# Kernel tuning notes

Measured on AMD Instinct MI355X. Metric: run time of the kernel, lower is better.

## Reference

```python
import jax, jax.numpy as jnp
import numpy as np
import math

B, D, N, H, NHEADS, NCLS = 4096, 256, 256, 1, 4, 10


def conv(x, w, b, stride, pad):
    y = jax.lax.conv_general_dilated(x, w, (stride, stride), [(pad, pad), (pad, pad)],
                                     dimension_numbers=('NCHW', 'OIHW', 'NCHW'))
    return y + b[None, :, None, None]


def cdist(z, c):
    # z: [B, D], c: [N, D] -> Euclidean distance [B, N]
    d2 = jnp.sum(z * z, -1)[:, None] + jnp.sum(c * c, -1)[None, :] - 2.0 * (z @ c.T)
    return jnp.sqrt(jnp.maximum(d2, 0.0))


def setup_inputs() -> dict:
    key = jax.random.key(0)
    ks = jax.random.split(key, 32)
    s = 0.02
    inp = {
        'x': jax.random.normal(ks[0], (B, 3, 32, 32), jnp.float32),
        'y': jax.random.randint(ks[1], (B,), 0, NCLS),
        'conv1_w': jax.random.normal(ks[2], (32, 3, 5, 5), jnp.float32) * s,
        'conv1_b': jnp.zeros((32,), jnp.float32),
        'conv2_w': jax.random.normal(ks[3], (64, 32, 3, 3), jnp.float32) * s,
        'conv2_b': jnp.zeros((64,), jnp.float32),
        'conv3_w': jax.random.normal(ks[4], (128, 64, 3, 3), jnp.float32) * s,
        'conv3_b': jnp.zeros((128,), jnp.float32),
        'conv4_w': jax.random.normal(ks[5], (256, 128, 3, 3), jnp.float32) * s,
        'conv4_b': jnp.zeros((256,), jnp.float32),
        'enc_w': jax.random.normal(ks[6], (256 * 8 * 8, D), jnp.float32) * s,
        'enc_b': jnp.zeros((D,), jnp.float32),
        'class_emb': jax.random.normal(ks[7], (NCLS, D), jnp.float32),
        'node_emb': jax.random.normal(ks[8], (N_NODES := 1, D), jnp.float32),
        'query_w': jax.random.normal(ks[9], (D, D), jnp.float32) * s,
        'query_b': jnp.zeros((D,), jnp.float32),
        'attn_w': jax.random.normal(ks[10], (D, D * NHEADS), jnp.float32) * s,
        'attn_b': jnp.zeros((D * NHEADS,), jnp.float32),
        'clf_w': jax.random.normal(ks[11], (D * NHEADS, NCLS), jnp.float32) * s,
        'clf_b': jnp.zeros((NCLS,), jnp.float32),
        'node_fc_w': jax.random.normal(ks[12], (D, D), jnp.float32) * s,
        'node_fc_b': jnp.zeros((D,), jnp.float32),
        'protos': jax.random.normal(ks[13], (N, D), jnp.float32),
        'grid_pos': jax.random.normal(ks[14], (N, D), jnp.float32),
        'temp_raw': jnp.array([math.log(0.95 / 0.05)], jnp.float32),
        'gate_logits': jnp.zeros((N,), jnp.float32),
    }
    return inp


def reference(x, y, conv1_w, conv1_b, conv2_w, conv2_b, conv3_w, conv3_b,
              conv4_w, conv4_b, enc_w, enc_b, class_emb, node_emb,
              query_w, query_b, attn_w, attn_b, clf_w, clf_b,
              node_fc_w, node_fc_b, protos, grid_pos, temp_raw, gate_logits):
    # shared encoder: conv stack -> flatten -> linear, 32x32 -> 8x8
    h1 = jax.nn.relu(conv(x, conv1_w, conv1_b, 2, 1))    # [B,32,15,15]
    h2 = jax.nn.relu(conv(h1, conv2_w, conv2_b, 2, 1))   # [B,64,8,8]
    h3 = jax.nn.relu(conv(h2, conv3_w, conv3_b, 1, 1))   # [B,128,8,8]
    h4 = jax.nn.relu(conv(h3, conv4_w, conv4_b, 1, 1))   # [B,256,8,8]
    z0 = h4.reshape(x.shape[0], -1) @ enc_w + enc_b      # [B,D]

    # Node: encoder_fc + SoftSOM (cdist + cdist -> softmax -> gate -> renorm -> blend)
    z = z0 @ node_fc_w + node_fc_b
    temp = jax.nn.sigmoid(temp_raw[0]) * (1.0 - 0.001) + 0.001
    d_total = cdist(z, protos) + cdist(z, grid_pos)      # [B,N]
    w = jax.nn.softmax(-d_total / temp, axis=-1) * jax.nn.sigmoid(gate_logits)[None, :]
    w = w / (w.sum(-1, keepdims=True) + 1e-8)
    blended = w @ protos                                 # [B,D]

    # node attention over n_nodes=1
    topo_stack = blended[:, None, :]                     # [B,1,D]
    query = class_emb[y] @ query_w + query_b             # [B,D]
    proj = (node_emb @ attn_w + attn_b).reshape(node_emb.shape[0], NHEADS, D)  # [n,h,D]
    attn_logits = jnp.einsum('bd,nhd->bhn', query, proj)
    attn_w_ = jax.nn.softmax(attn_logits, axis=-1)
    fused = jnp.einsum('bhn,bnd->bhd', attn_w_, topo_stack).reshape(x.shape[0], NHEADS * D)
    logits = fused @ clf_w + clf_b                       # [B,10]
    return logits
```

## Files before the change

### kernel.cpp

```cpp
#include <hip/hip_runtime.h>
#include <math.h>

#define TPB 256

typedef __attribute__((ext_vector_type(8))) short bf16x8;
typedef __attribute__((ext_vector_type(4))) float f32x4;
typedef __attribute__((ext_vector_type(2))) float f32x2;

#define OFF_PN2   0
#define OFF_GN2   256
#define OFF_GATE  512
#define OFF_TEMP  768
#define OFF_WEFF  1024
#define OFF_W1T   3584
#define OFF_W2T_BYTES 737280ul
#define OFF_W3T_BYTES 786432ul
#define OFF_W4T_BYTES 983040ul
#define OFF_EWT_BYTES 2097152ul
#define OFF_NFWT_BYTES 10485760ul
#define OFF_PJD_BYTES  10616832ul
#define OFF_GJD_BYTES  10747904ul
#define OFF_PTB_BYTES  10878976ul
#define OFF_A_BYTES   12582912ul
#define OFF_B_BYTES   (OFF_A_BYTES + 67108864ul)
#define OFF_Z0_BYTES  (OFF_B_BYTES + 33554432ul)

__device__ __forceinline__ float bf2f(ushort u) {
  return __uint_as_float(((unsigned)u) << 16);
}
__device__ __forceinline__ ushort f2bf(float f) {
  unsigned x = __float_as_uint(f);
  return (ushort)((x + 0x7fffu + ((x >> 16) & 1u)) >> 16);
}
__device__ __forceinline__ unsigned pack2(float a, float b) {
  return (unsigned)f2bf(a) | ((unsigned)f2bf(b) << 16);
}

__device__ __forceinline__ void gload_lds16(const ushort* g, ushort* l) {
  __builtin_amdgcn_global_load_lds(
      (const __attribute__((address_space(1))) unsigned int*)g,
      (__attribute__((address_space(3))) unsigned int*)l, 16, 0, 0);
}

__device__ __forceinline__ float block_sum(float v, float* red) {
  #pragma unroll
  for (int off = 32; off > 0; off >>= 1) v += __shfl_down(v, off, 64);
  int wid = threadIdx.x >> 6;
  __syncthreads();
  if ((threadIdx.x & 63) == 0) red[wid] = v;
  __syncthreads();
  return red[0] + red[1] + red[2] + red[3];
}

__global__ void __launch_bounds__(256) k_setup(const float* __restrict__ protos,
    const float* __restrict__ gridp, const float* __restrict__ gate_logits,
    const float* __restrict__ temp_raw, const float* __restrict__ clf_w,
    float* __restrict__ ws, float* __restrict__ z0) {
  __shared__ float red[4];
  int b = blockIdx.x, t = threadIdx.x;
  #pragma unroll
  for (int u = 0; u < 16; ++u) z0[(size_t)u*65536 + b*256 + t] = 0.f;
  float pv = protos[b*256 + t];
  float gv = gridp [b*256 + t];
  float sp = block_sum(pv*pv, red);
  float sg = block_sum(gv*gv, red);
  if (t == 0) {
    ws[OFF_PN2 + b] = sp;
    ws[OFF_GN2 + b] = sg;
    ws[OFF_GATE + b] = 1.f/(1.f + expf(-gate_logits[b]));
  }
  if (b == 0) {
    for (int i = t; i < 2560; i += TPB) {
      int d = i/10, c = i%10;
      ws[OFF_WEFF + i] = clf_w[d*10+c] + clf_w[(256+d)*10+c]
                       + clf_w[(512+d)*10+c] + clf_w[(768+d)*10+c];
    }
    if (t == 0) {
      float s = 1.f/(1.f + expf(-temp_raw[0]));
      ws[OFF_TEMP] = s*(1.f - 0.001f) + 0.001f;
    }
  }
}

__global__ void __launch_bounds__(256) k_prep(const float* __restrict__ w1,
    const float* __restrict__ w2, const float* __restrict__ w3,
    const float* __restrict__ w4, float* __restrict__ w1t,
    ushort* __restrict__ w2t, ushort* __restrict__ w3t, ushort* __restrict__ w4t) {
  int idx = blockIdx.x*256 + threadIdx.x;
  if (idx < 2400) {
    int tap = idx >> 5, oc = idx & 31;
    w1t[idx] = w1[oc*75 + tap];
  }
  if (idx < 18432) {
    int tap = idx >> 11, r = idx & 2047, oc = r >> 5, ic = r & 31;
    w2t[idx] = f2bf(w2[oc*288 + ic*9 + tap]);
  }
  if (idx < 73728) {
    int tap = idx >> 13, r = idx & 8191, oc = r >> 6, ic = r & 63;
    w3t[idx] = f2bf(w3[oc*576 + ic*9 + tap]);
  }
  if (idx < 294912) {
    int tap = idx >> 15, r = idx & 32767, oc = r >> 7, ic = r & 127;
    w4t[idx] = f2bf(w4[oc*1152 + ic*9 + tap]);
  }
}

__global__ void __launch_bounds__(256) k_prep2(const float* __restrict__ nfw,
    const float* __restrict__ protos, const float* __restrict__ gridp,
    ushort* __restrict__ nfwt, ushort* __restrict__ pjd,
    ushort* __restrict__ gjd, ushort* __restrict__ ptb) {
  int idx = blockIdx.x*256 + threadIdx.x;
  int a = idx >> 8, b = idx & 255;
  nfwt[idx] = f2bf(nfw[b*256 + a]);
  pjd [idx] = f2bf(protos[idx]);
  gjd [idx] = f2bf(gridp[idx]);
  ptb [idx] = f2bf(protos[b*256 + a]);
}

__global__ void __launch_bounds__(256) k_trans(const float* __restrict__ ew,
    ushort* __restrict__ ewt) {
  __shared__ float tile[64][65];
  int kb = blockIdx.x, nb = blockIdx.y, t = threadIdx.x;
  #pragma unroll
  for (int i = 0; i < 16; ++i) {
    int idx = t + i*256, k = idx >> 6, n = idx & 63;
    tile[k][n] = ew[(size_t)(kb*64 + k)*256 + nb*64 + n];
  }
  __syncthreads();
  #pragma unroll
  for (int i = 0; i < 16; ++i) {
    int idx = t + i*256, n = idx >> 6, k = idx & 63;
    ewt[(size_t)(nb*64 + n)*16384 + kb*64 + k] = f2bf(tile[k][n]);
  }
}

__global__ void __launch_bounds__(256) k_conv12(const float* __restrict__ x,
    const float* __restrict__ w1t, const float* __restrict__ b1,
    const ushort* __restrict__ w2t, const float* __restrict__ b2,
    ushort* __restrict__ h2c) {
  __shared__ ushort xs[17*17*40];
  int b = blockIdx.x, t = threadIdx.x;
  for (int i = t; i < 5780; i += TPB) ((unsigned*)xs)[i] = 0u;
  const float* xb = x + (size_t)b*3072;

  if (t < 225) {
    int oy = t/15, ox = t%15;
    f32x2 acc[16];
    #pragma unroll
    for (int o = 0; o < 16; ++o) acc[o] = *(const f32x2*)&b1[2*o];
    for (int ic = 0; ic < 3; ++ic) {
      const int icb = ic*1024;
      #pragma unroll
      for (int ky = 0; ky < 5; ++ky) {
        int iy = 2*oy - 1 + ky;
        bool rok = (unsigned)iy < 32u;
        int rbase = icb + (rok ? iy*32 : 0);
        #pragma unroll
        for (int kx = 0; kx < 5; ++kx) {
          int ix = 2*ox - 1 + kx;
          bool ok = rok && ((unsigned)ix < 32u);
          float xv = xb[rbase + (ok ? ix : 0)];
          xv = ok ? xv : 0.f;
          f32x2 xv2 = {xv, xv};
          const float* wrow = &w1t[(ic*25 + ky*5 + kx)*32];
          #pragma unroll
          for (int g = 0; g < 8; ++g) {
            f32x2 wlo = {wrow[4*g+0], wrow[4*g+1]};
            f32x2 whi = {wrow[4*g+2], wrow[4*g+3]};
            acc[2*g]   += xv2*wlo;
            acc[2*g+1] += xv2*whi;
          }
        }
      }
    }
    unsigned pk[16];
    #pragma unroll
    for (int g = 0; g < 16; ++g)
      pk[g] = pack2(fmaxf(acc[g].x, 0.f), fmaxf(acc[g].y, 0.f));
    ushort* cell = &xs[((oy+1)*17 + (ox+1))*40];
    #pragma unroll
    for (int q = 0; q < 4; ++q) *(uint4*)(cell + q*8) = ((uint4*)pk)[q];
  }
  __syncthreads();

  const int lane = t & 63, w = t >> 6;
  const int quad = lane >> 4, row16 = lane & 15;
  f32x4 acc2[4];
  #pragma unroll
  for (int mt = 0; mt < 4; ++mt) acc2[mt] = (f32x4)0.f;
  #pragma unroll
  for (int ky = 0; ky < 3; ++ky)
    #pragma unroll
    for (int kx = 0; kx < 3; ++kx) {
      int tap = ky*3 + kx;
      bf16x8 bf = *(const bf16x8*)&w2t[tap*2048 + (w*16 + row16)*32 + quad*8];
      #pragma unroll
      for (int mt = 0; mt < 4; ++mt) {
        int px = mt*16 + row16;
        int iy = 2*(px >> 3) + ky, ix = 2*(px & 7) + kx;
        bf16x8 af = *(const bf16x8*)&xs[(iy*17 + ix)*40 + quad*8];
        acc2[mt] = __builtin_amdgcn_mfma_f32_16x16x32_bf16(bf, af, acc2[mt], 0, 0, 0);
      }
    }
  float4 bb = *(const float4*)&b2[w*16 + quad*4];
  #pragma unroll
  for (int mt = 0; mt < 4; ++mt) {
    int px = mt*16 + row16;
    uint2 dd;
    dd.x = pack2(fmaxf(acc2[mt][0] + bb.x, 0.f), fmaxf(acc2[mt][1] + bb.y, 0.f));
    dd.y = pack2(fmaxf(acc2[mt][2] + bb.z, 0.f), fmaxf(acc2[mt][3] + bb.w, 0.f));
    *(uint2*)&h2c[(size_t)b*4096 + px*64 + w*16 + quad*4] = dd;
  }
}

__global__ void __launch_bounds__(256, 2) k_conv34(const ushort* __restrict__ h2c,
    const float* __restrict__ b3, const float* __restrict__ b4,
    const ushort* __restrict__ w3t, const ushort* __restrict__ w4t,
    ushort* __restrict__ h4c, int img_base) {
  __shared__ ushort buf[2*8704];
  ushort* xp  = buf;
  ushort* h3p = buf;
  const int bl = blockIdx.x, t = threadIdx.x;
  #pragma unroll
  for (int u = 0; u < 4; ++u) {
    int i = t + u*256;
    int img = i >> 9, r = i & 511, px = r >> 3, icq = r & 7;
    bf16x8 v = *(const bf16x8*)&h2c[(size_t)(img_base + bl*2 + img)*4096 + px*64 + icq*8];
    *(bf16x8*)&xp[img*4608 + px*72 + icq*8] = v;
  }
  __syncthreads();

  const int lane = t & 63, oq = t >> 6;
  const int quad = lane >> 4, row16 = lane & 15;
  const bf16x8 zr = (bf16x8)(short)0;
  int aoy[8], aox[8], ioff3[8], ioff4[8];
  #pragma unroll
  for (int mt = 0; mt < 8; ++mt) {
    int px = (mt & 3)*16 + row16;
    aoy[mt] = px >> 3; aox[mt] = px & 7;
    ioff3[mt] = (mt >> 2)*4608;
    ioff4[mt] = (mt >> 2)*8704;
  }

  f32x4 c3[8][2];
  #pragma unroll
  for (int mt = 0; mt < 8; ++mt) { c3[mt][0] = (f32x4)0.f; c3[mt][1] = (f32x4)0.f; }
  const ushort* wb3 = w3t + (oq*32 + row16)*64 + quad*8;
  bf16x8 r3a = *(const bf16x8*)(wb3);
  bf16x8 r3b = *(const bf16x8*)(wb3 + 1024);
  for (int tap = 0; tap < 9; ++tap, wb3 += 8192) {
    int ky = tap/3, kx = tap - 3*ky;
    int ab[8]; bool vv[8];
    #pragma unroll
    for (int mt = 0; mt < 8; ++mt) {
      int iy = aoy[mt] + ky - 1, ix = aox[mt] + kx - 1;
      vv[mt] = ((unsigned)iy < 8u) && ((unsigned)ix < 8u);
      int pxv = vv[mt] ? (iy*8 + ix) : 0;
      ab[mt] = ioff3[mt] + pxv*72 + quad*8;
    }
    #pragma unroll
    for (int ks = 0; ks < 2; ++ks) {
      const ushort* wn = wb3 + ((ks == 1) ? 8192 : 32);
      bf16x8 n0 = *(const bf16x8*)(wn);
      bf16x8 n1 = *(const bf16x8*)(wn + 1024);
      #pragma unroll
      for (int mt = 0; mt < 8; ++mt) {
        bf16x8 ax = *(const bf16x8*)&xp[ab[mt] + ks*32];
        ax = vv[mt] ? ax : zr;
        c3[mt][0] = __builtin_amdgcn_mfma_f32_16x16x32_bf16(r3a, ax, c3[mt][0], 0, 0, 0);
        c3[mt][1] = __builtin_amdgcn_mfma_f32_16x16x32_bf16(r3b, ax, c3[mt][1], 0, 0, 0);
      }
      r3a = n0; r3b = n1;
    }
  }
  __syncthreads();
  #pragma unroll
  for (int nt = 0; nt < 2; ++nt) {
    float4 bb = *(const float4*)&b3[oq*32 + nt*16 + quad*4];
    #pragma unroll
    for (int mt = 0; mt < 8; ++mt) {
      int px = (mt & 3)*16 + row16;
      uint2 dd;
      dd.x = pack2(fmaxf(c3[mt][nt][0] + bb.x, 0.f), fmaxf(c3[mt][nt][1] + bb.y, 0.f));
      dd.y = pack2(fmaxf(c3[mt][nt][2] + bb.z, 0.f), fmaxf(c3[mt][nt][3] + bb.w, 0.f));
      *(uint2*)&h3p[ioff4[mt] + px*136 + oq*32 + nt*16 + quad*4] = dd;
    }
  }
  __syncthreads();

  f32x4 c4[8][4];
  #pragma unroll
  for (int mt = 0; mt < 8; ++mt)
    #pragma unroll
    for (int nt = 0; nt < 4; ++nt) c4[mt][nt] = (f32x4)0.f;
  const ushort* wb4 = w4t + (oq*64 + row16)*128 + quad*8;
  bf16x8 r4[4];
  #pragma unroll
  for (int nt = 0; nt < 4; ++nt) r4[nt] = *(const bf16x8*)(wb4 + nt*2048);
  for (int tap = 0; tap < 9; ++tap, wb4 += 32768) {
    int ky = tap/3, kx = tap - 3*ky;
    int ab[8]; bool vv[8];
    #pragma unroll
    for (int mt = 0; mt < 8; ++mt) {
      int iy = aoy[mt] + ky - 1, ix = aox[mt] + kx - 1;
      vv[mt] = ((unsigned)iy < 8u) && ((unsigned)ix < 8u);
      int pxv = vv[mt] ? (iy*8 + ix) : 0;
      ab[mt] = ioff4[mt] + pxv*136 + quad*8;
    }
    #pragma unroll
    for (int ks = 0; ks < 4; ++ks) {
      const ushort* wn = wb4 + ((ks == 3) ? 32768 : (ks + 1)*32);
      bf16x8 nx[4];
      #pragma unroll
      for (int nt = 0; nt < 4; ++nt) nx[nt] = *(const bf16x8*)(wn + nt*2048);
      #pragma unroll
      for (int mt = 0; mt < 8; ++mt) {
        bf16x8 ax = *(const bf16x8*)&h3p[ab[mt] + ks*32];
        ax = vv[mt] ? ax : zr;
        #pragma unroll
        for (int nt = 0; nt < 4; ++nt)
          c4[mt][nt] = __builtin_amdgcn_mfma_f32_16x16x32_bf16(ax, r4[nt], c4[mt][nt], 0, 0, 0);
      }
      #pragma unroll
      for (int nt = 0; nt < 4; ++nt) r4[nt] = nx[nt];
    }
  }
  #pragma unroll
  for (int nt = 0; nt < 4; ++nt) {
    int oc = oq*64 + nt*16 + row16;
    float bv = b4[oc];
    #pragma unroll
    for (int mt = 0; mt < 8; ++mt) {
      int ig = bl*2 + (mt >> 2);
      int px0 = (mt & 3)*16 + quad*4;
      uint2 dd;
      dd.x = pack2(fmaxf(c4[mt][nt][0] + bv, 0.f), fmaxf(c4[mt][nt][1] + bv, 0.f));
      dd.y = pack2(fmaxf(c4[mt][nt][2] + bv, 0.f), fmaxf(c4[mt][nt][3] + bv, 0.f));
      *(uint2*)&h4c[(size_t)ig*16384 + oc*64 + px0] = dd;
    }
  }
}

__global__ void __launch_bounds__(256) k_enc(const ushort* __restrict__ h4c,
    const ushort* __restrict__ ewt, float* __restrict__ z0, int img_base) {
  __shared__ ushort a_s[128*64];
  __shared__ ushort b_s[128*64];
  const int t = threadIdx.x, bx = blockIdx.x;
  const int slice = bx & 15;
  const int mb = (bx >> 4) & 15;
  const int nb = bx >> 8;
  const int M0 = mb*128, N0 = nb*128;
  const int kbase = slice*1024;
  const int lane = t & 63, wv = t >> 6;
  const int quad = lane >> 4, row16 = lane & 15;
  const int mrow0 = (wv & 1)*64, ncol0 = (wv >> 1)*64;
  const int sr = lane >> 3, sp = lane & 7;

  f32x4 acc[4][4];
  #pragma unroll
  for (int mt = 0; mt < 4; ++mt)
    #pragma unroll
    for (int nt = 0; nt < 4; ++nt) acc[mt][nt] = (f32x4)0.f;

  for (int kt = 0; kt < 16; ++kt) {
    const int k0 = kbase + kt*64;
    __syncthreads();
    #pragma unroll
    for (int u = 0; u < 4; ++u) {
      int r = wv*32 + u*8 + sr;
      int c = sp ^ (r & 7);
      gload_lds16(&h4c[(size_t)(M0 + r)*16384 + k0 + c*8], &a_s[(wv*32 + u*8)*64]);
      gload_lds16(&ewt[(size_t)(N0 + r)*16384 + k0 + c*8], &b_s[(wv*32 + u*8)*64]);
    }
    __syncthreads();
    #pragma unroll
    for (int ks = 0; ks < 2; ++ks) {
      bf16x8 af[4], bf[4];
      #pragma unroll
      for (int mt = 0; mt < 4; ++mt) {
        int r = mrow0 + mt*16 + row16;
        int p = (ks*4 + quad) ^ (r & 7);
        af[mt] = *(const bf16x8*)&a_s[r*64 + p*8];
      }
      #pragma unroll
      for (int nt = 0; nt < 4; ++nt) {
        int r = ncol0 + nt*16 + row16;
        int p = (ks*4 + quad) ^ (r & 7);
        bf[nt] = *(const bf16x8*)&b_s[r*64 + p*8];
      }
      #pragma unroll
      for (int mt = 0; mt < 4; ++mt)
        #pragma unroll
        for (int nt = 0; nt < 4; ++nt)
          acc[mt][nt] = __builtin_amdgcn_mfma_f32_16x16x32_bf16(af[mt], bf[nt], acc[mt][nt], 0, 0, 0);
    }
  }
  #pragma unroll
  for (int mt = 0; mt < 4; ++mt) {
    int mrow = M0 + mrow0 + mt*16 + quad*4;
    #pragma unroll
    for (int nt = 0; nt < 4; ++nt) {
      int col = N0 + ncol0 + nt*16 + row16;
      #pragma unroll
      for (int r = 0; r < 4; ++r)
        atomicAdd(&z0[(size_t)(img_base + mrow + r)*256 + col], acc[mt][nt][r]);
    }
  }
}

__global__ void __launch_bounds__(256) k_post2(const float* __restrict__ z0,
    const float* __restrict__ enc_b, const float* __restrict__ nfb,
    const ushort* __restrict__ nfwt, const ushort* __restrict__ pjd,
    const ushort* __restrict__ gjd, const ushort* __restrict__ ptb,
    const float* __restrict__ ws, const float* __restrict__ clf_b,
    float* __restrict__ out) {
  __shared__ ushort zin[16*264];
  __shared__ ushort zS [16*264];
  __shared__ float  Df [16*264];
  __shared__ ushort wS [16*264];
  __shared__ float  z2s[16];
  const int t = threadIdx.x, bx = blockIdx.x;
  const int img0 = bx*16;
  #pragma unroll
  for (int u = 0; u < 16; ++u) {
    int i = t + u*256;
    int im = i >> 8, d = i & 255;
    zin[im*264 + d] = f2bf(z0[(size_t)(img0 + im)*256 + d] + enc_b[d]);
  }
  __syncthreads();

  const int lane = t & 63, w = t >> 6;
  const int quad = lane >> 4, row16 = lane & 15;
  const int n0 = w*64;

  f32x4 zC[4];
  #pragma unroll
  for (int nt = 0; nt < 4; ++nt) zC[nt] = (f32x4)0.f;
  #pragma unroll
  for (int ks = 0; ks < 8; ++ks) {
    bf16x8 az = *(const bf16x8*)&zin[row16*264 + ks*32 + quad*8];
    #pragma unroll
    for (int nt = 0; nt < 4; ++nt) {
      bf16x8 bw = *(const bf16x8*)&nfwt[(n0 + nt*16 + row16)*256 + ks*32 + quad*8];
      zC[nt] = __builtin_amdgcn_mfma_f32_16x16x32_bf16(az, bw, zC[nt], 0, 0, 0);
    }
  }
  #pragma unroll
  for (int nt = 0; nt < 4; ++nt) {
    int n = n0 + nt*16 + row16;
    float nb = nfb[n];
    #pragma unroll
    for (int r = 0; r < 4; ++r)
      zS[(quad*4 + r)*264 + n] = f2bf(zC[nt][r] + nb);
  }
  __syncthreads();

  {
    int im = t >> 4, jg = t & 15;
    float s = 0.f;
    #pragma unroll
    for (int q = 0; q < 16; ++q) {
      float v = bf2f(zS[im*264 + jg + 16*q]);
      s += v*v;
    }
    #pragma unroll
    for (int off = 8; off; off >>= 1) s += __shfl_xor(s, off, 16);
    if (jg == 0) z2s[im] = s;
  }
  __syncthreads();

  f32x4 dpC[4], dgC[4];
  #pragma unroll
  for (int nt = 0; nt < 4; ++nt) { dpC[nt] = (f32x4)0.f; dgC[nt] = (f32x4)0.f; }
  #pragma unroll
  for (int ks = 0; ks < 8; ++ks) {
    bf16x8 az = *(const bf16x8*)&zS[row16*264 + ks*32 + quad*8];
    #pragma unroll
    for (int nt = 0; nt < 4; ++nt) {
      int j = n0 + nt*16 + row16;
      bf16x8 bp = *(const bf16x8*)&pjd[j*256 + ks*32 + quad*8];
      bf16x8 bg = *(const bf16x8*)&gjd[j*256 + ks*32 + quad*8];
      dpC[nt] = __builtin_amdgcn_mfma_f32_16x16x32_bf16(az, bp, dpC[nt], 0, 0, 0);
      dgC[nt] = __builtin_amdgcn_mfma_f32_16x16x32_bf16(az, bg, dgC[nt], 0, 0, 0);
    }
  }
  {
    float temp = ws[OFF_TEMP];
    #pragma unroll
    for (int nt = 0; nt < 4; ++nt) {
      int j = n0 + nt*16 + row16;
      float pn = ws[OFF_PN2 + j], gn = ws[OFF_GN2 + j];
      #pragma unroll
      for (int r = 0; r < 4; ++r) {
        int im = quad*4 + r;
        float z2 = z2s[im];
        float d2p = z2 + pn - 2.f*dpC[nt][r];
        float d2g = z2 + gn - 2.f*dgC[nt][r];
        float l = -(sqrtf(fmaxf(d2p, 0.f)) + sqrtf(fmaxf(d2g, 0.f)))/temp;
        Df[im*264 + j] = l;
      }
    }
  }
  __syncthreads();

  {
    int im = t >> 4, jg = t & 15;
    float m = -1e30f;
    #pragma unroll
    for (int q = 0; q < 16; ++q) m = fmaxf(m, Df[im*264 + jg + 16*q]);
    #pragma unroll
    for (int off = 8; off; off >>= 1) m = fmaxf(m, __shfl_xor(m, off, 16));
    float E = 0.f, S = 0.f, ev[16], gv[16];
    #pragma unroll
    for (int q = 0; q < 16; ++q) {
      int j = jg + 16*q;
      float e = expf(Df[im*264 + j] - m);
      float g = ws[OFF_GATE + j];
      ev[q] = e; gv[q] = g;
      E += e; S += e*g;
    }
    #pragma unroll
    for (int off = 8; off; off >>= 1) {
      E += __shfl_xor(E, off, 16);
      S += __shfl_xor(S, off, 16);
    }
    float inv = 1.f/(S + 1e-8f*E);
    #pragma unroll
    for (int q = 0; q < 16; ++q)
      wS[im*264 + jg + 16*q] = f2bf(ev[q]*gv[q]*inv);
  }
  __syncthreads();

  f32x4 blC[4];
  #pragma unroll
  for (int nt = 0; nt < 4; ++nt) blC[nt] = (f32x4)0.f;
  #pragma unroll
  for (int ks = 0; ks < 8; ++ks) {
    bf16x8 aw = *(const bf16x8*)&wS[row16*264 + ks*32 + quad*8];
    #pragma unroll
    for (int nt = 0; nt < 4; ++nt) {
      bf16x8 bp = *(const bf16x8*)&ptb[(n0 + nt*16 + row16)*256 + ks*32 + quad*8];
      blC[nt] = __builtin_amdgcn_mfma_f32_16x16x32_bf16(aw, bp, blC[nt], 0, 0, 0);
    }
  }
  #pragma unroll
  for (int nt = 0; nt < 4; ++nt) {
    int d = n0 + nt*16 + row16;
    #pragma unroll
    for (int r = 0; r < 4; ++r)
      Df[(quad*4 + r)*264 + d] = blC[nt][r];
  }
  __syncthreads();

  if (t < 160) {
    int im = t/10, c = t - im*10;
    float s = clf_b[c];
    for (int d = 0; d < 256; ++d)
      s += Df[im*264 + d]*ws[OFF_WEFF + d*10 + c];
    out[(size_t)(img0 + im)*10 + c] = s;
  }
}

extern "C" void kernel_launch(void* const* d_in, const int* in_sizes, int n_in,
                              void* d_out, int out_size, void* d_ws, size_t ws_size,
                              hipStream_t stream) {
  (void)in_sizes; (void)n_in; (void)out_size; (void)ws_size;
  const float* x      = (const float*)d_in[0];
  const float* c1w    = (const float*)d_in[2];
  const float* c1b    = (const float*)d_in[3];
  const float* c2w    = (const float*)d_in[4];
  const float* c2b    = (const float*)d_in[5];
  const float* c3w    = (const float*)d_in[6];
  const float* c3b    = (const float*)d_in[7];
  const float* c4w    = (const float*)d_in[8];
  const float* c4b    = (const float*)d_in[9];
  const float* encw   = (const float*)d_in[10];
  const float* encb   = (const float*)d_in[11];
  const float* clfw   = (const float*)d_in[18];
  const float* clfb   = (const float*)d_in[19];
  const float* nfw    = (const float*)d_in[20];
  const float* nfb    = (const float*)d_in[21];
  const float* protos = (const float*)d_in[22];
  const float* gridp  = (const float*)d_in[23];
  const float* traw   = (const float*)d_in[24];
  const float* gatel  = (const float*)d_in[25];

  float*  ws   = (float*)d_ws;
  float*  w1t  = ws + OFF_W1T;
  ushort* w2t  = (ushort*)((char*)d_ws + OFF_W2T_BYTES);
  ushort* w3t  = (ushort*)((char*)d_ws + OFF_W3T_BYTES);
  ushort* w4t  = (ushort*)((char*)d_ws + OFF_W4T_BYTES);
  ushort* ewt  = (ushort*)((char*)d_ws + OFF_EWT_BYTES);
  ushort* nfwt = (ushort*)((char*)d_ws + OFF_NFWT_BYTES);
  ushort* pjd  = (ushort*)((char*)d_ws + OFF_PJD_BYTES);
  ushort* gjd  = (ushort*)((char*)d_ws + OFF_GJD_BYTES);
  ushort* ptb  = (ushort*)((char*)d_ws + OFF_PTB_BYTES);
  ushort* h4c  = (ushort*)((char*)d_ws + OFF_A_BYTES);
  ushort* h2c  = (ushort*)((char*)d_ws + OFF_B_BYTES);
  float*  z0   = (float*) ((char*)d_ws + OFF_Z0_BYTES);
  float*  out  = (float*)d_out;

  hipLaunchKernelGGL(k_setup, dim3(256),  dim3(TPB), 0, stream, protos, gridp, gatel, traw, clfw, ws, z0);
  hipLaunchKernelGGL(k_prep,  dim3(1152), dim3(TPB), 0, stream, c1w, c2w, c3w, c4w, w1t, w2t, w3t, w4t);
  hipLaunchKernelGGL(k_prep2, dim3(256),  dim3(TPB), 0, stream, nfw, protos, gridp, nfwt, pjd, gjd, ptb);
  hipLaunchKernelGGL(k_trans, dim3(256, 4), dim3(TPB), 0, stream, encw, ewt);
  hipLaunchKernelGGL(k_conv12, dim3(4096), dim3(TPB), 0, stream, x, w1t, c1b, w2t, c2b, h2c);
  for (int c = 0; c < 2; ++c) {
    hipLaunchKernelGGL(k_conv34, dim3(1024), dim3(TPB), 0, stream,
                       h2c, c3b, c4b, w3t, w4t, h4c, c*2048);
    hipLaunchKernelGGL(k_enc, dim3(512), dim3(TPB), 0, stream, h4c, ewt, z0, c*2048);
  }
  hipLaunchKernelGGL(k_post2, dim3(256), dim3(TPB), 0, stream,
                     z0, encb, nfb, nfwt, pjd, gjd, ptb, ws, clfb, out);
}
```

Baseline: 560.7 us.

## Rewrite conv3/conv4 kernel with 32x32 MFMA, 512 threads and XOR-swizzled LDS

The fused conv3+conv4 kernel now runs 512 threads per block, with each group of four waves handling one image. It switches from 16x16x32 to 32x32x16 bf16 MFMA tiles and replaces the padded LDS layout with an XOR swizzle. The goal is higher occupancy, fewer MFMA issues and less wasted LDS, avoiding bank conflicts without padding. The larger block and 16-wide accumulators raise register pressure under the launch bound, and each wave now reloads its own weight fragments from global memory.

```diff
diff --git a/kernel.cpp b/kernel.cpp
--- a/kernel.cpp
+++ b/kernel.cpp
@@ -5,6 +5,7 @@
 
 typedef __attribute__((ext_vector_type(8))) short bf16x8;
 typedef __attribute__((ext_vector_type(4))) float f32x4;
+typedef __attribute__((ext_vector_type(16))) float f32x16;
 typedef __attribute__((ext_vector_type(2))) float f32x2;
 
 #define OFF_PN2   0
@@ -213,130 +214,136 @@
   }
 }
 
-__global__ void __launch_bounds__(256, 2) k_conv34(const ushort* __restrict__ h2c,
+__global__ void __launch_bounds__(512, 4) k_conv34(const ushort* __restrict__ h2c,
     const float* __restrict__ b3, const float* __restrict__ b4,
     const ushort* __restrict__ w3t, const ushort* __restrict__ w4t,
     ushort* __restrict__ h4c, int img_base) {
-  __shared__ ushort buf[2*8704];
+  __shared__ ushort buf[16384];
   ushort* xp  = buf;
   ushort* h3p = buf;
   const int bl = blockIdx.x, t = threadIdx.x;
-  #pragma unroll
-  for (int u = 0; u < 4; ++u) {
-    int i = t + u*256;
-    int img = i >> 9, r = i & 511, px = r >> 3, icq = r & 7;
-    bf16x8 v = *(const bf16x8*)&h2c[(size_t)(img_base + bl*2 + img)*4096 + px*64 + icq*8];
-    *(bf16x8*)&xp[img*4608 + px*72 + icq*8] = v;
-  }
-  __syncthreads();
-
-  const int lane = t & 63, oq = t >> 6;
-  const int quad = lane >> 4, row16 = lane & 15;
+
+  #pragma unroll
+  for (int u = 0; u < 2; ++u) {
+    int i = t + u*512;
+    int im = i >> 9, px = (i >> 3) & 63, icg = i & 7;
+    bf16x8 v = *(const bf16x8*)&h2c[(size_t)(img_base + bl*2 + im)*4096 + px*64 + icg*8];
+    *(bf16x8*)&xp[im*4096 + px*64 + ((icg ^ (px & 7)) << 3)] = v;
+  }
+  __syncthreads();
+
+  const int lane = t & 63, w = t >> 6;
+  const int half = lane >> 5, ln = lane & 31;
+  const int img = w >> 2;
+  const int xbase3 = img*4096, xbase4 = img*8192;
   const bf16x8 zr = (bf16x8)(short)0;
-  int aoy[8], aox[8], ioff3[8], ioff4[8];
-  #pragma unroll
-  for (int mt = 0; mt < 8; ++mt) {
-    int px = (mt & 3)*16 + row16;
-    aoy[mt] = px >> 3; aox[mt] = px & 7;
-    ioff3[mt] = (mt >> 2)*4608;
-    ioff4[mt] = (mt >> 2)*8704;
-  }
-
-  f32x4 c3[8][2];
-  #pragma unroll
-  for (int mt = 0; mt < 8; ++mt) { c3[mt][0] = (f32x4)0.f; c3[mt][1] = (f32x4)0.f; }
-  const ushort* wb3 = w3t + (oq*32 + row16)*64 + quad*8;
-  bf16x8 r3a = *(const bf16x8*)(wb3);
-  bf16x8 r3b = *(const bf16x8*)(wb3 + 1024);
-  for (int tap = 0; tap < 9; ++tap, wb3 += 8192) {
+
+  const int ocb3 = (w & 3) * 32;
+  f32x16 a3[2];
+  a3[0] = (f32x16)0.f; a3[1] = (f32x16)0.f;
+  const ushort* w3b = w3t + (ocb3 + ln)*64 + half*8;
+  bf16x8 wc3 = *(const bf16x8*)w3b;
+  for (int tap = 0; tap < 9; ++tap) {
     int ky = tap/3, kx = tap - 3*ky;
-    int ab[8]; bool vv[8];
-    #pragma unroll
-    for (int mt = 0; mt < 8; ++mt) {
-      int iy = aoy[mt] + ky - 1, ix = aox[mt] + kx - 1;
-      vv[mt] = ((unsigned)iy < 8u) && ((unsigned)ix < 8u);
-      int pxv = vv[mt] ? (iy*8 + ix) : 0;
-      ab[mt] = ioff3[mt] + pxv*72 + quad*8;
-    }
-    #pragma unroll
-    for (int ks = 0; ks < 2; ++ks) {
-      const ushort* wn = wb3 + ((ks == 1) ? 8192 : 32);
-      bf16x8 n0 = *(const bf16x8*)(wn);
-      bf16x8 n1 = *(const bf16x8*)(wn + 1024);
-      #pragma unroll
-      for (int mt = 0; mt < 8; ++mt) {
-        bf16x8 ax = *(const bf16x8*)&xp[ab[mt] + ks*32];
-        ax = vv[mt] ? ax : zr;
-        c3[mt][0] = __builtin_amdgcn_mfma_f32_16x16x32_bf16(r3a, ax, c3[mt][0], 0, 0, 0);
-        c3[mt][1] = __builtin_amdgcn_mfma_f32_16x16x32_bf16(r3b, ax, c3[mt][1], 0, 0, 0);
-      }
-      r3a = n0; r3b = n1;
-    }
-  }
-  __syncthreads();
-  #pragma unroll
-  for (int nt = 0; nt < 2; ++nt) {
-    float4 bb = *(const float4*)&b3[oq*32 + nt*16 + quad*4];
-    #pragma unroll
-    for (int mt = 0; mt < 8; ++mt) {
-      int px = (mt & 3)*16 + row16;
+    int pxv[2]; bool vv[2];
+    #pragma unroll
+    for (int p = 0; p < 2; ++p) {
+      int px = p*32 + ln;
+      int iy = (px >> 3) + ky - 1, ix = (px & 7) + kx - 1;
+      vv[p] = ((unsigned)iy < 8u) && ((unsigned)ix < 8u);
+      pxv[p] = vv[p] ? (iy*8 + ix) : 0;
+    }
+    #pragma unroll
+    for (int ks = 0; ks < 4; ++ks) {
+      const ushort* wn = (ks < 3) ? (w3b + tap*8192 + (ks+1)*16)
+                                  : (w3b + (tap+1)*8192);
+      bf16x8 wnx = *(const bf16x8*)wn;
+      #pragma unroll
+      for (int p = 0; p < 2; ++p) {
+        int icg = ks*2 + half;
+        bf16x8 xf = *(const bf16x8*)&xp[xbase3 + pxv[p]*64 + ((icg ^ (pxv[p] & 7)) << 3)];
+        xf = vv[p] ? xf : zr;
+        a3[p] = __builtin_amdgcn_mfma_f32_32x32x16_bf16(wc3, xf, a3[p], 0, 0, 0);
+      }
+      wc3 = wnx;
+    }
+  }
+  __syncthreads();
+  #pragma unroll
+  for (int q = 0; q < 4; ++q) {
+    float4 bb = *(const float4*)&b3[ocb3 + 8*q + 4*half];
+    int ocg = (ocb3 >> 3) + q;
+    #pragma unroll
+    for (int p = 0; p < 2; ++p) {
+      int px = p*32 + ln;
       uint2 dd;
-      dd.x = pack2(fmaxf(c3[mt][nt][0] + bb.x, 0.f), fmaxf(c3[mt][nt][1] + bb.y, 0.f));
-      dd.y = pack2(fmaxf(c3[mt][nt][2] + bb.z, 0.f), fmaxf(c3[mt][nt][3] + bb.w, 0.f));
-      *(uint2*)&h3p[ioff4[mt] + px*136 + oq*32 + nt*16 + quad*4] = dd;
-    }
-  }
-  __syncthreads();
-
-  f32x4 c4[8][4];
-  #pragma unroll
-  for (int mt = 0; mt < 8; ++mt)
-    #pragma unroll
-    for (int nt = 0; nt < 4; ++nt) c4[mt][nt] = (f32x4)0.f;
-  const ushort* wb4 = w4t + (oq*64 + row16)*128 + quad*8;
-  bf16x8 r4[4];
-  #pragma unroll
-  for (int nt = 0; nt < 4; ++nt) r4[nt] = *(const bf16x8*)(wb4 + nt*2048);
-  for (int tap = 0; tap < 9; ++tap, wb4 += 32768) {
+      dd.x = pack2(fmaxf(a3[p][4*q+0] + bb.x, 0.f), fmaxf(a3[p][4*q+1] + bb.y, 0.f));
+      dd.y = pack2(fmaxf(a3[p][4*q+2] + bb.z, 0.f), fmaxf(a3[p][4*q+3] + bb.w, 0.f));
+      *(uint2*)&h3p[xbase4 + px*128 + ((ocg ^ (px & 15)) << 3) + 4*half] = dd;
+    }
+  }
+  __syncthreads();
+
+  const int ocb4 = (w & 3) * 64;
+  f32x16 a4[2][2];
+  a4[0][0] = (f32x16)0.f; a4[0][1] = (f32x16)0.f;
+  a4[1][0] = (f32x16)0.f; a4[1][1] = (f32x16)0.f;
+  const ushort* w4b = w4t + half*8;
+  const int wo0 = (ocb4 + ln)*128, wo1 = wo0 + 32*128;
+  bf16x8 wc4[2];
+  wc4[0] = *(const bf16x8*)(w4b + wo0);
+  wc4[1] = *(const bf16x8*)(w4b + wo1);
+  for (int tap = 0; tap < 9; ++tap) {
     int ky = tap/3, kx = tap - 3*ky;
-    int ab[8]; bool vv[8];
-    #pragma unroll
-    for (int mt = 0; mt < 8; ++mt) {
-      int iy = aoy[mt] + ky - 1, ix = aox[mt] + kx - 1;
-      vv[mt] = ((unsigned)iy < 8u) && ((unsigned)ix < 8u);
-      int pxv = vv[mt] ? (iy*8 + ix) : 0;
-      ab[mt] = ioff4[mt] + pxv*136 + quad*8;
-    }
-    #pragma unroll
-    for (int ks = 0; ks < 4; ++ks) {
-      const ushort* wn = wb4 + ((ks == 3) ? 32768 : (ks + 1)*32);
-      bf16x8 nx[4];
-      #pragma unroll
-      for (int nt = 0; nt < 4; ++nt) nx[nt] = *(const bf16x8*)(wn + nt*2048);
-      #pragma unroll
-      for (int mt = 0; mt < 8; ++mt) {
-        bf16x8 ax = *(const bf16x8*)&h3p[ab[mt] + ks*32];
-        ax = vv[mt] ? ax : zr;
+    int pxv[2]; bool vv[2];
+    #pragma unroll
+    for (int p = 0; p < 2; ++p) {
+      int px = p*32 + ln;
+      int iy = (px >> 3) + ky - 1, ix = (px & 7) + kx - 1;
+      vv[p] = ((unsigned)iy < 8u) && ((unsigned)ix < 8u);
+      pxv[p] = vv[p] ? (iy*8 + ix) : 0;
+    }
+    #pragma unroll
+    for (int ks = 0; ks < 8; ++ks) {
+      bf16x8 wnx[2];
+      {
+        const ushort* wnA = (ks < 7) ? (w4b + tap*32768 + wo0 + (ks+1)*16)
+                                     : (w4b + (tap+1)*32768 + wo0);
+        const ushort* wnB = (ks < 7) ? (w4b + tap*32768 + wo1 + (ks+1)*16)
+                                     : (w4b + (tap+1)*32768 + wo1);
+        wnx[0] = *(const bf16x8*)wnA;
+        wnx[1] = *(const bf16x8*)wnB;
+      }
+      bf16x8 xf[2];
+      #pragma unroll
+      for (int p = 0; p < 2; ++p) {
+        int icg = ks*2 + half;
+        xf[p] = *(const bf16x8*)&h3p[xbase4 + pxv[p]*128 + ((icg ^ (pxv[p] & 15)) << 3)];
+        xf[p] = vv[p] ? xf[p] : zr;
+      }
+      #pragma unroll
+      for (int o = 0; o < 2; ++o)
         #pragma unroll
-        for (int nt = 0; nt < 4; ++nt)
-          c4[mt][nt] = __builtin_amdgcn_mfma_f32_16x16x32_bf16(ax, r4[nt], c4[mt][nt], 0, 0, 0);
-      }
-      #pragma unroll
-      for (int nt = 0; nt < 4; ++nt) r4[nt] = nx[nt];
-    }
-  }
-  #pragma unroll
-  for (int nt = 0; nt < 4; ++nt) {
-    int oc = oq*64 + nt*16 + row16;
+        for (int p = 0; p < 2; ++p)
+          a4[o][p] = __builtin_amdgcn_mfma_f32_32x32x16_bf16(xf[p], wc4[o], a4[o][p], 0, 0, 0);
+      wc4[0] = wnx[0]; wc4[1] = wnx[1];
+    }
+  }
+  const int ig = img_base + bl*2 + img;
+  #pragma unroll
+  for (int o = 0; o < 2; ++o) {
+    int oc = ocb4 + o*32 + ln;
     float bv = b4[oc];
     #pragma unroll
-    for (int mt = 0; mt < 8; ++mt) {
-      int ig = bl*2 + (mt >> 2);
-      int px0 = (mt & 3)*16 + quad*4;
-      uint2 dd;
-      dd.x = pack2(fmaxf(c4[mt][nt][0] + bv, 0.f), fmaxf(c4[mt][nt][1] + bv, 0.f));
-      dd.y = pack2(fmaxf(c4[mt][nt][2] + bv, 0.f), fmaxf(c4[mt][nt][3] + bv, 0.f));
-      *(uint2*)&h4c[(size_t)ig*16384 + oc*64 + px0] = dd;
+    for (int p = 0; p < 2; ++p) {
+      #pragma unroll
+      for (int q = 0; q < 4; ++q) {
+        int px0 = p*32 + 8*q + 4*half;
+        uint2 dd;
+        dd.x = pack2(fmaxf(a4[o][p][4*q+0] + bv, 0.f), fmaxf(a4[o][p][4*q+1] + bv, 0.f));
+        dd.y = pack2(fmaxf(a4[o][p][4*q+2] + bv, 0.f), fmaxf(a4[o][p][4*q+3] + bv, 0.f));
+        *(uint2*)&h4c[(size_t)ig*16384 + oc*64 + px0] = dd;
+      }
     }
   }
 }
@@ -606,7 +613,7 @@
   hipLaunchKernelGGL(k_trans, dim3(256, 4), dim3(TPB), 0, stream, encw, ewt);
   hipLaunchKernelGGL(k_conv12, dim3(4096), dim3(TPB), 0, stream, x, w1t, c1b, w2t, c2b, h2c);
   for (int c = 0; c < 2; ++c) {
-    hipLaunchKernelGGL(k_conv34, dim3(1024), dim3(TPB), 0, stream,
+    hipLaunchKernelGGL(k_conv34, dim3(1024), dim3(512), 0, stream,
                        h2c, c3b, c4b, w3t, w4t, h4c, c*2048);
     hipLaunchKernelGGL(k_enc, dim3(512), dim3(TPB), 0, stream, h4c, ewt, z0, c*2048);
   }
```

Result: slower. 698.7 us (+24.6%).
